# Performance work log

Hardware: AMD Instinct MI355X
Metric: run time of the kernel (lower is better)

The kernel has to match this reference:

```python
import jax, jax.numpy as jnp
import numpy as np

N, D = 512, 256          # n candidates, span_emb_size
R = 4                    # num relation types / etypes
FF = 512                 # mention_linker_ffnn_size, depth 1
L = 2                    # ieg_bignn_hidden_layers
DH = D // 2              # GraphConvolution output size


def setup_inputs() -> dict:
    key = jax.random.key(0)
    ks = jax.random.split(key, 12)
    s = lambda fan_in: 1.0 / np.sqrt(fan_in)
    return {
        "candidate_embs": jax.random.normal(ks[0], (N, D), jnp.float32),
        # relation scorer FFNN: 3D -> FF -> R
        "W_sc0": jax.random.normal(ks[1], (3 * D, FF), jnp.float32) * s(3 * D),
        "b_sc0": jnp.zeros((FF,), jnp.float32),
        "W_sc1": jax.random.normal(ks[2], (FF, R), jnp.float32) * s(FF),
        "b_sc1": jnp.zeros((R,), jnp.float32),
        # BiGCN: per-layer, per-relation fw/bw GraphConvolution D -> D//2
        "W_fw": jax.random.normal(ks[3], (L, R, D, DH), jnp.float32) * s(D),
        "b_fw": jnp.zeros((L, R, DH), jnp.float32),
        "W_bw": jax.random.normal(ks[4], (L, R, D, DH), jnp.float32) * s(D),
        "b_bw": jnp.zeros((L, R, DH), jnp.float32),
        # per-layer linear1: D -> D
        "W_lin": jax.random.normal(ks[5], (L, D, D), jnp.float32) * s(D),
        "b_lin": jnp.zeros((L, D), jnp.float32),
    }


def reference(candidate_embs, W_sc0, b_sc0, W_sc1, b_sc1,
              W_fw, b_fw, W_bw, b_bw, W_lin, b_lin):
    n, d = candidate_embs.shape
    # --- get_pair_embs: [n, n, 3d] = cat(src, target, src*target) ---
    src = jnp.broadcast_to(candidate_embs[None, :, :], (n, n, d))   # row i varies j
    tgt = jnp.broadcast_to(candidate_embs[:, None, :], (n, n, d))
    pair = jnp.concatenate([src, tgt, src * tgt], axis=-1)          # [n, n, 3d]
    # --- relation scorer FFNN (ReLU hidden, dropout=0 at inference) ---
    h = jax.nn.relu(jnp.einsum('ijk,kf->ijf', pair, W_sc0) + b_sc0)
    scores = jnp.einsum('ijf,fr->ijr', h, W_sc1) + b_sc1            # [n, n, R]
    probs = jax.nn.softmax(scores, axis=-1)
    # --- adjs_from_preds: detach, zero diagonal; bw = fw^T ---
    probs = jax.lax.stop_gradient(probs)
    A = jnp.moveaxis(probs, -1, 0)                                   # [R, n, n]
    eye = jnp.eye(n, dtype=bool)
    A = jnp.where(eye[None, :, :], 0.0, A)
    AT = jnp.swapaxes(A, 1, 2)
    # --- BiGCN: L layers of multi-relation bi-directional GCN ---
    x = candidate_embs
    for l in range(L):
        sup_fw = jnp.einsum('nd,rde->rne', x, W_fw[l])               # [R, n, DH]
        sup_bw = jnp.einsum('nd,rde->rne', x, W_bw[l])
        fw = jnp.einsum('rij,rje->rie', A, sup_fw) + b_fw[l][:, None, :]
        bw = jnp.einsum('rij,rje->rie', AT, sup_bw) + b_bw[l][:, None, :]
        outs = jnp.concatenate([bw, fw], axis=-1)                    # [R, n, D]
        x = jax.nn.relu(outs.sum(axis=0)) @ W_lin[l] + b_lin[l] + x  # residual
    return x
```

## Files before the change

kernel.cpp:

```cpp
#include <hip/hip_runtime.h>
#include <hip/hip_bf16.h>

using f32x4  = __attribute__((ext_vector_type(4))) float;
using bf16x8 = __attribute__((ext_vector_type(8))) short;

__device__ __forceinline__ unsigned short f2bf(float f) {
    union { __hip_bfloat16 h; unsigned short u; } cv;
    cv.h = __float2bfloat16(f);
    return cv.u;
}
__device__ __forceinline__ unsigned int pack2bf(float lo, float hi) {
    float2 t; t.x = lo; t.y = hi;
    union { __hip_bfloat162 h; unsigned int u; } cv;
    cv.h = __float22bfloat162_rn(t);
    return cv.u;
}

__global__ __launch_bounds__(512) void prep_uv_kernel(
        const float* __restrict__ E, const float* __restrict__ Wsc0, const float* __restrict__ bsc0,
        const float* __restrict__ Wfw, const float* __restrict__ bfw,
        const float* __restrict__ Wbw, const float* __restrict__ bbw,
        const float* __restrict__ Wlin,
        unsigned short* __restrict__ E16, unsigned short* __restrict__ W0p,
        unsigned short* __restrict__ WcatT, unsigned short* __restrict__ WlinT,
        float* __restrict__ bsumS, float* __restrict__ Upk, float* __restrict__ V) {
    __shared__ float sE[8][256];
    if (blockIdx.x < 512) {
        const int NE = 131072, NW0 = 131072, NCAT = 524288, NLIN = 131072;
        const int total = NE + NW0 + NCAT + NLIN + 512;
        for (int idx = blockIdx.x * 512 + threadIdx.x; idx < total; idx += 512 * 512) {
            int t = idx;
            if (t < NE) { E16[t] = f2bf(E[t]); continue; }
            t -= NE;
            if (t < NW0) {
                int e = t & 7, lane = (t >> 3) & 63, kk = (t >> 9) & 7, nb = (t >> 12) & 3, w = (t >> 14) & 7;
                int fcol = w * 64 + nb * 16 + (lane & 15);
                int k = kk * 32 + (lane >> 4) * 8 + e;
                W0p[t] = f2bf(Wsc0[(512 + k) * 512 + fcol]);
                continue;
            }
            t -= NW0;
            if (t < NCAT) {
                int e = t & 127, k = (t >> 7) & 255, r = (t >> 15) & 3, d = (t >> 17) & 1, l = t >> 18;
                const float* src = (d == 0) ? Wfw : Wbw;
                float v = src[((l * 4 + r) * 256 + k) * 128 + e];
                WcatT[(l * 1024 + d * 512 + r * 128 + e) * 256 + k] = f2bf(v);
                continue;
            }
            t -= NCAT;
            if (t < NLIN) {
                int d = t & 255, f = (t >> 8) & 255, l = t >> 16;
                WlinT[(l * 256 + d) * 256 + f] = f2bf(Wlin[(l * 256 + f) * 256 + d]);
                continue;
            }
            t -= NLIN;
            {
                int f = t & 255, l = t >> 8;
                float s = 0.f;
                if (f < 128) { for (int r = 0; r < 4; ++r) s += bbw[(l * 4 + r) * 128 + f]; }
                else         { for (int r = 0; r < 4; ++r) s += bfw[(l * 4 + r) * 128 + (f - 128)]; }
                bsumS[l * 256 + f] = s;
            }
        }
    } else {
        int j0 = (blockIdx.x - 512) * 8;
        int tid = threadIdx.x;
        for (int t = tid; t < 2048; t += 512) sE[t >> 8][t & 255] = E[j0 * 256 + t];
        __syncthreads();
        int f = tid;
        float u[8] = {0,0,0,0,0,0,0,0}, v[8] = {0,0,0,0,0,0,0,0};
        for (int k = 0; k < 256; ++k) {
            float wa = Wsc0[k * 512 + f];
            float wb = Wsc0[(256 + k) * 512 + f];
#pragma unroll
            for (int jj = 0; jj < 8; ++jj) { u[jj] += sE[jj][k] * wa; v[jj] += sE[jj][k] * wb; }
        }
        float b0f = bsc0[f];
        int w = f >> 6, nb = (f >> 4) & 3, l15 = f & 15;
#pragma unroll
        for (int jj = 0; jj < 8; ++jj) {
            int j = j0 + jj;
            int j0b = j >> 6, mb = (j >> 4) & 3, lane = ((j >> 2) & 3) * 16 + l15, reg = j & 3;
            Upk[((((j0b * 8 + w) * 4 + mb) * 4 + nb) * 64 + lane) * 4 + reg] = u[jj] + b0f;
            V[j * 512 + f] = v[jj];
        }
    }
}

__global__ __launch_bounds__(512, 4) void pair_kernel(
    const float* __restrict__ E, const unsigned short* __restrict__ W0p,
    const float* __restrict__ Upk, const float* __restrict__ V,
    const float* __restrict__ W1, const float* __restrict__ b1,
    unsigned short* __restrict__ A16) {

    __shared__ unsigned short prodL[64 * 256];
    __shared__ float partial2[64 * 36];
    __shared__ float scoresL[64 * 4];

    const int i = blockIdx.x;
    const int j0b = blockIdx.y;
    const int j0 = j0b * 64;
    const int tid = threadIdx.x;
    const int lane = tid & 63;
    const int w = tid >> 6;
    const int l15 = lane & 15, l4 = lane >> 4;

    float Vv[4];
#pragma unroll
    for (int nb = 0; nb < 4; ++nb) Vv[nb] = V[i * 512 + w * 64 + nb * 16 + l15];
    const float4* Up4 = (const float4*)Upk;
    f32x4 acc[4][4];
#pragma unroll
    for (int mb = 0; mb < 4; ++mb)
#pragma unroll
        for (int nb = 0; nb < 4; ++nb) {
            float4 uv_ = Up4[(((j0b * 8 + w) * 4 + mb) * 4 + nb) * 64 + lane];
            acc[mb][nb][0] = uv_.x + Vv[nb];
            acc[mb][nb][1] = uv_.y + Vv[nb];
            acc[mb][nb][2] = uv_.z + Vv[nb];
            acc[mb][nb][3] = uv_.w + Vv[nb];
        }

    {
        int m = tid >> 3;
        const float4* ej = (const float4*)(E + (j0 + m) * 256);
        const float4* ei = (const float4*)(E + i * 256);
        char* base = (char*)prodL;
#pragma unroll
        for (int c = 0; c < 8; ++c) {
            int q = (tid & 7) + c * 8;
            float4 a = ej[q], b = ei[q];
            uint2 val;
            val.x = pack2bf(a.x * b.x, a.y * b.y);
            val.y = pack2bf(a.z * b.z, a.w * b.w);
            int byteoff = m * 512 + ((q * 8) ^ ((m & 7) << 4));
            *(uint2*)(base + byteoff) = val;
        }
    }
    __syncthreads();

    const char* pbase = (const char*)prodL;
    const bf16x8* Wp8 = (const bf16x8*)W0p;
#pragma unroll
    for (int kk = 0; kk < 8; ++kk) {
        bf16x8 afr[4], bfr[4];
#pragma unroll
        for (int mb = 0; mb < 4; ++mb) {
            int row = mb * 16 + l15;
            int off = row * 512 + ((kk * 64 + l4 * 16) ^ ((row & 7) << 4));
            afr[mb] = *(const bf16x8*)(pbase + off);
        }
#pragma unroll
        for (int nb = 0; nb < 4; ++nb)
            bfr[nb] = Wp8[((w * 4 + nb) * 8 + kk) * 64 + lane];
#pragma unroll
        for (int mb = 0; mb < 4; ++mb)
#pragma unroll
            for (int nb = 0; nb < 4; ++nb)
                acc[mb][nb] = __builtin_amdgcn_mfma_f32_16x16x32_bf16(afr[mb], bfr[nb], acc[mb][nb], 0, 0, 0);
    }

    float4 w1v[4];
#pragma unroll
    for (int nb = 0; nb < 4; ++nb) w1v[nb] = *(const float4*)(W1 + (w * 64 + nb * 16 + l15) * 4);
#pragma unroll
    for (int mb = 0; mb < 4; ++mb) {
        float s2[4][4];
#pragma unroll
        for (int reg = 0; reg < 4; ++reg) {
            s2[reg][0] = 0.f; s2[reg][1] = 0.f; s2[reg][2] = 0.f; s2[reg][3] = 0.f;
#pragma unroll
            for (int nb = 0; nb < 4; ++nb) {
                float h = fmaxf(acc[mb][nb][reg], 0.f);
                s2[reg][0] += h * w1v[nb].x;
                s2[reg][1] += h * w1v[nb].y;
                s2[reg][2] += h * w1v[nb].z;
                s2[reg][3] += h * w1v[nb].w;
            }
        }
#pragma unroll
        for (int reg = 0; reg < 4; ++reg)
#pragma unroll
            for (int r = 0; r < 4; ++r) {
                float vs = s2[reg][r];
                vs += __shfl_xor(vs, 1);
                vs += __shfl_xor(vs, 2);
                vs += __shfl_xor(vs, 4);
                vs += __shfl_xor(vs, 8);
                s2[reg][r] = vs;
            }
#pragma unroll
        for (int reg = 0; reg < 4; ++reg)
#pragma unroll
            for (int r = 0; r < 4; ++r)
                if (l15 == r)
                    partial2[(mb * 16 + l4 * 4 + reg) * 36 + r * 9 + w] = s2[reg][r];
    }
    __syncthreads();
    if (tid < 256) {
        int m = tid >> 2, r = tid & 3;
        float sc = b1[r];
#pragma unroll
        for (int p = 0; p < 8; ++p) sc += partial2[m * 36 + r * 9 + p];
        scoresL[m * 4 + r] = sc;
    }
    __syncthreads();
    if (tid < 64) {
        int m = tid, j = j0 + m;
        float s0 = scoresL[m * 4 + 0], s1 = scoresL[m * 4 + 1];
        float sA = scoresL[m * 4 + 2], sB = scoresL[m * 4 + 3];
        float mx = fmaxf(fmaxf(s0, s1), fmaxf(sA, sB));
        float e0 = __expf(s0 - mx), e1 = __expf(s1 - mx), e2 = __expf(sA - mx), e3 = __expf(sB - mx);
        float inv = 1.f / (e0 + e1 + e2 + e3);
        float p_[4] = {e0 * inv, e1 * inv, e2 * inv, e3 * inv};
        if (j == i) { p_[0] = p_[1] = p_[2] = p_[3] = 0.f; }
#pragma unroll
        for (int r = 0; r < 4; ++r)
            A16[(r * 512 + i) * 512 + j] = f2bf(p_[r]);
    }
}

template<int K>
__device__ __forceinline__ void stageP(unsigned short* lds, const unsigned short* g, int ldg, int tid) {
    constexpr int SLOTS = K / 8;
#pragma unroll
    for (int it = 0; it < (32 * SLOTS) / 256; ++it) {
        int u = it * 256 + tid;
        int row = u / SLOTS, slot = u % SLOTS;
        uint4 v = *(const uint4*)(g + row * ldg + slot * 8);
        *(uint4*)((char*)lds + row * (K * 2) + ((slot * 16) ^ ((row & 7) << 4))) = v;
    }
}
template<int K>
__device__ __forceinline__ bf16x8 fragP(const unsigned short* lds, int row, int kc, int l4) {
    return *(const bf16x8*)((const char*)lds + row * (K * 2) + ((((kc * 4 + l4) * 16) ^ ((row & 7) << 4))));
}

__global__ __launch_bounds__(256) void c1_kernel(const unsigned short* __restrict__ WcatT,
                                                 const unsigned short* __restrict__ x16,
                                                 unsigned short* __restrict__ supT,
                                                 const unsigned short* __restrict__ A16,
                                                 unsigned short* __restrict__ AT16, int l) {
    __shared__ unsigned short lA[32 * 256], lB[32 * 256];
    int tid = threadIdx.x;
    if (blockIdx.y >= 16) {
        auto t = (unsigned short(*)[65])lA;
        int job = (blockIdx.y - 16) * 32 + blockIdx.x;
        int r = job >> 6, ty = (job >> 3) & 7, tx = job & 7;
        const unsigned short* src = A16 + (r * 512 + ty * 64) * 512 + tx * 64;
        unsigned short* dst = AT16 + (r * 512 + tx * 64) * 512 + ty * 64;
#pragma unroll
        for (int it = 0; it < 2; ++it) {
            int u = it * 256 + tid, row = u >> 3, c8 = (u & 7) * 8;
            uint4 v = *(const uint4*)(src + row * 512 + c8);
            const unsigned short* p = (const unsigned short*)&v;
#pragma unroll
            for (int e = 0; e < 8; ++e) t[c8 + e][row] = p[e];
        }
        __syncthreads();
#pragma unroll
        for (int it = 0; it < 2; ++it) {
            int u = it * 256 + tid, row = u >> 3, c8 = (u & 7) * 8;
            uint4 v; unsigned short* p = (unsigned short*)&v;
#pragma unroll
            for (int e = 0; e < 8; ++e) p[e] = t[row][c8 + e];
            *(uint4*)(dst + row * 512 + c8) = v;
        }
        return;
    }
    int c0 = blockIdx.x * 32, jt0 = blockIdx.y * 32;
    int lane = tid & 63, w = tid >> 6;
    int wr = (w >> 1) * 16, wc = (w & 1) * 16;
    int l15 = lane & 15, l4 = lane >> 4;
    stageP<256>(lA, WcatT + l * 262144 + c0 * 256, 256, tid);
    stageP<256>(lB, x16 + jt0 * 256, 256, tid);
    __syncthreads();
    f32x4 a0 = {0.f,0.f,0.f,0.f}, a1 = {0.f,0.f,0.f,0.f};
#pragma unroll
    for (int kc = 0; kc < 8; kc += 2) {
        a0 = __builtin_amdgcn_mfma_f32_16x16x32_bf16(fragP<256>(lA, wr + l15, kc, l4),
                                                     fragP<256>(lB, wc + l15, kc, l4), a0, 0, 0, 0);
        a1 = __builtin_amdgcn_mfma_f32_16x16x32_bf16(fragP<256>(lA, wr + l15, kc + 1, l4),
                                                     fragP<256>(lB, wc + l15, kc + 1, l4), a1, 0, 0, 0);
    }
    f32x4 acc = a0 + a1;
#pragma unroll
    for (int reg = 0; reg < 4; ++reg) {
        int c = c0 + wr + l4 * 4 + reg;
        int j = jt0 + wc + l15;
        supT[c * 512 + j] = f2bf(acc[reg]);
    }
}

__global__ __launch_bounds__(256) void c2_kernel(const unsigned short* __restrict__ A16,
                                                 const unsigned short* __restrict__ AT16,
                                                 const unsigned short* __restrict__ supT,
                                                 const float* __restrict__ bsumS,
                                                 unsigned short* __restrict__ relS, int l) {
    __shared__ unsigned short lA[32 * 512], lB[32 * 512];
    int i0 = blockIdx.x * 32, f0 = blockIdx.y * 32;
    bool bw = (f0 < 128);
    const unsigned short* Am = bw ? AT16 : A16;
    int e0 = bw ? f0 : (f0 - 128);
    int tid = threadIdx.x, lane = tid & 63, w = tid >> 6;
    int wr = (w >> 1) * 16, wc = (w & 1) * 16;
    int l15 = lane & 15, l4 = lane >> 4;
    f32x4 a0 = {0.f,0.f,0.f,0.f}, a1 = {0.f,0.f,0.f,0.f};
    for (int r = 0; r < 4; ++r) {
        if (r) __syncthreads();
        stageP<512>(lA, Am + (r * 512 + i0) * 512, 512, tid);
        stageP<512>(lB, supT + ((bw ? 512 : 0) + r * 128 + e0) * 512, 512, tid);
        __syncthreads();
#pragma unroll
        for (int kc = 0; kc < 16; kc += 2) {
            a0 = __builtin_amdgcn_mfma_f32_16x16x32_bf16(fragP<512>(lA, wr + l15, kc, l4),
                                                         fragP<512>(lB, wc + l15, kc, l4), a0, 0, 0, 0);
            a1 = __builtin_amdgcn_mfma_f32_16x16x32_bf16(fragP<512>(lA, wr + l15, kc + 1, l4),
                                                         fragP<512>(lB, wc + l15, kc + 1, l4), a1, 0, 0, 0);
        }
    }
    f32x4 acc = a0 + a1;
#pragma unroll
    for (int reg = 0; reg < 4; ++reg) {
        int ii = i0 + wr + l4 * 4 + reg;
        int f = f0 + wc + l15;
        relS[ii * 256 + f] = f2bf(fmaxf(acc[reg] + bsumS[l * 256 + f], 0.f));
    }
}

__global__ __launch_bounds__(256) void c3_kernel(const unsigned short* __restrict__ relS,
                                                 const unsigned short* __restrict__ WlinT,
                                                 const float* __restrict__ blin,
                                                 const float* __restrict__ xold,
                                                 float* __restrict__ xnew,
                                                 unsigned short* __restrict__ x16out, int l) {
    __shared__ unsigned short lA[32 * 256], lB[32 * 256];
    int i0 = blockIdx.x * 32, d0 = blockIdx.y * 32;
    int tid = threadIdx.x, lane = tid & 63, w = tid >> 6;
    int wr = (w >> 1) * 16, wc = (w & 1) * 16;
    int l15 = lane & 15, l4 = lane >> 4;
    stageP<256>(lA, relS + i0 * 256, 256, tid);
    stageP<256>(lB, WlinT + l * 65536 + d0 * 256, 256, tid);
    __syncthreads();
    f32x4 a0 = {0.f,0.f,0.f,0.f}, a1 = {0.f,0.f,0.f,0.f};
#pragma unroll
    for (int kc = 0; kc < 8; kc += 2) {
        a0 = __builtin_amdgcn_mfma_f32_16x16x32_bf16(fragP<256>(lA, wr + l15, kc, l4),
                                                     fragP<256>(lB, wc + l15, kc, l4), a0, 0, 0, 0);
        a1 = __builtin_amdgcn_mfma_f32_16x16x32_bf16(fragP<256>(lA, wr + l15, kc + 1, l4),
                                                     fragP<256>(lB, wc + l15, kc + 1, l4), a1, 0, 0, 0);
    }
    f32x4 acc = a0 + a1;
#pragma unroll
    for (int reg = 0; reg < 4; ++reg) {
        int ii = i0 + wr + l4 * 4 + reg;
        int dd = d0 + wc + l15;
        float vv = acc[reg] + blin[l * 256 + dd] + xold[ii * 256 + dd];
        xnew[ii * 256 + dd] = vv;
        x16out[ii * 256 + dd] = f2bf(vv);
    }
}

extern "C" void kernel_launch(void* const* d_in, const int* in_sizes, int n_in,
                              void* d_out, int out_size, void* d_ws, size_t ws_size,
                              hipStream_t stream) {
    const float* E    = (const float*)d_in[0];
    const float* Wsc0 = (const float*)d_in[1];
    const float* bsc0 = (const float*)d_in[2];
    const float* Wsc1 = (const float*)d_in[3];
    const float* bsc1 = (const float*)d_in[4];
    const float* Wfw  = (const float*)d_in[5];
    const float* bfw  = (const float*)d_in[6];
    const float* Wbw  = (const float*)d_in[7];
    const float* bbw  = (const float*)d_in[8];
    const float* Wlin = (const float*)d_in[9];
    const float* blin = (const float*)d_in[10];
    float* out = (float*)d_out;

    char* ws = (char*)d_ws;
    size_t off = 0;
    unsigned short* E16   = (unsigned short*)(ws + off); off += 512 * 256 * 2;
    unsigned short* W0p   = (unsigned short*)(ws + off); off += 512 * 256 * 2;
    unsigned short* WcatT = (unsigned short*)(ws + off); off += 2 * 1024 * 256 * 2;
    unsigned short* WlinT = (unsigned short*)(ws + off); off += 2 * 256 * 256 * 2;
    float* bsumS          = (float*)(ws + off);          off += 2 * 256 * 4;
    float* Upk            = (float*)(ws + off);          off += 512 * 512 * 4;
    float* V              = (float*)(ws + off);          off += 512 * 512 * 4;
    unsigned short* A16   = (unsigned short*)(ws + off); off += 4 * 512 * 512 * 2;
    unsigned short* AT16  = (unsigned short*)(ws + off); off += 4 * 512 * 512 * 2;
    unsigned short* supT  = (unsigned short*)(ws + off); off += 1024 * 512 * 2;
    unsigned short* relS  = (unsigned short*)(ws + off); off += 512 * 256 * 2;
    float* xf1            = (float*)(ws + off);          off += 512 * 256 * 4;
    unsigned short* x16_1 = (unsigned short*)(ws + off); off += 512 * 256 * 2;

    prep_uv_kernel<<<576, 512, 0, stream>>>(E, Wsc0, bsc0, Wfw, bfw, Wbw, bbw, Wlin,
                                            E16, W0p, WcatT, WlinT, bsumS, Upk, V);
    pair_kernel<<<dim3(512, 8), 512, 0, stream>>>(E, W0p, Upk, V, Wsc1, bsc1, A16);

    for (int l = 0; l < 2; ++l) {
        const unsigned short* xin16 = (l == 0) ? E16 : x16_1;
        const float* xoldf = (l == 0) ? E : xf1;
        float* xout = (l == 0) ? xf1 : out;
        c1_kernel<<<dim3(32, (l == 0) ? 24 : 16), 256, 0, stream>>>(WcatT, xin16, supT, A16, AT16, l);
        c2_kernel<<<dim3(16, 8), 256, 0, stream>>>(A16, AT16, supT, bsumS, relS, l);
        c3_kernel<<<dim3(16, 8), 256, 0, stream>>>(relS, WlinT, blin, xoldf, xout, x16_1, l);
    }
    (void)in_sizes; (void)n_in; (void)out_size; (void)ws_size;
}
```

Measured before the change: 223.9 us.

## Use MFMA for scorer output layer, bf16 U, split-K c2 with reduction in c3

The pair kernel's second FFNN layer (hidden to 4 relations) now runs on MFMA instead of scalar FMAs and shuffle reductions. Hidden activations are written to LDS as bf16, and W1 is padded into a 16-column bf16 fragment layout. The precomputed U term is stored as bf16 to halve its load traffic, and pair_kernel launch bounds are lowered to 3 waves/SIMD. The GCN aggregation kernel c2 is split across relation and K-half into 8 fp32 partial slices for more blocks, with c3 summing the slices, adding bias and ReLU. The costs are extra global traffic for the partials, more bf16 rounding, and added syncs in pair_kernel.

```diff
diff --git a/kernel.cpp b/kernel.cpp
--- a/kernel.cpp
+++ b/kernel.cpp
@@ -15,19 +15,24 @@
     cv.h = __float22bfloat162_rn(t);
     return cv.u;
 }
+__device__ __forceinline__ float bf2f(unsigned short u) {
+    return __uint_as_float((unsigned)u << 16);
+}
 
 __global__ __launch_bounds__(512) void prep_uv_kernel(
         const float* __restrict__ E, const float* __restrict__ Wsc0, const float* __restrict__ bsc0,
+        const float* __restrict__ Wsc1,
         const float* __restrict__ Wfw, const float* __restrict__ bfw,
         const float* __restrict__ Wbw, const float* __restrict__ bbw,
         const float* __restrict__ Wlin,
         unsigned short* __restrict__ E16, unsigned short* __restrict__ W0p,
         unsigned short* __restrict__ WcatT, unsigned short* __restrict__ WlinT,
-        float* __restrict__ bsumS, float* __restrict__ Upk, float* __restrict__ V) {
+        float* __restrict__ bsumS, unsigned short* __restrict__ Upk,
+        float* __restrict__ V, unsigned short* __restrict__ W1p) {
     __shared__ float sE[8][256];
     if (blockIdx.x < 512) {
-        const int NE = 131072, NW0 = 131072, NCAT = 524288, NLIN = 131072;
-        const int total = NE + NW0 + NCAT + NLIN + 512;
+        const int NE = 131072, NW0 = 131072, NCAT = 524288, NLIN = 131072, NW1P = 8192;
+        const int total = NE + NW0 + NCAT + NLIN + NW1P + 512;
         for (int idx = blockIdx.x * 512 + threadIdx.x; idx < total; idx += 512 * 512) {
             int t = idx;
             if (t < NE) { E16[t] = f2bf(E[t]); continue; }
@@ -54,6 +59,14 @@
                 continue;
             }
             t -= NLIN;
+            if (t < NW1P) {
+                int e = t & 7, lane = (t >> 3) & 63, kk = t >> 9;
+                int f = kk * 32 + (lane >> 4) * 8 + e;
+                int r = lane & 15;
+                W1p[t] = (r < 4) ? f2bf(Wsc1[f * 4 + r]) : (unsigned short)0;
+                continue;
+            }
+            t -= NW1P;
             {
                 int f = t & 255, l = t >> 8;
                 float s = 0.f;
@@ -80,26 +93,26 @@
 #pragma unroll
         for (int jj = 0; jj < 8; ++jj) {
             int j = j0 + jj;
-            int j0b = j >> 6, mb = (j >> 4) & 3, lane = ((j >> 2) & 3) * 16 + l15, reg = j & 3;
-            Upk[((((j0b * 8 + w) * 4 + mb) * 4 + nb) * 64 + lane) * 4 + reg] = u[jj] + b0f;
+            int jt = j >> 6, mb = (j >> 4) & 3, lane = ((j >> 2) & 3) * 16 + l15, reg = j & 3;
+            Upk[(((((jt * 8 + w) * 4 + mb) * 4 + nb) * 64 + lane) * 4 + reg)] = f2bf(u[jj] + b0f);
             V[j * 512 + f] = v[jj];
         }
     }
 }
 
-__global__ __launch_bounds__(512, 4) void pair_kernel(
+__global__ __launch_bounds__(512, 3) void pair_kernel(
     const float* __restrict__ E, const unsigned short* __restrict__ W0p,
-    const float* __restrict__ Upk, const float* __restrict__ V,
-    const float* __restrict__ W1, const float* __restrict__ b1,
+    const unsigned short* __restrict__ Upk, const float* __restrict__ V,
+    const unsigned short* __restrict__ W1p, const float* __restrict__ b1,
     unsigned short* __restrict__ A16) {
 
     __shared__ unsigned short prodL[64 * 256];
-    __shared__ float partial2[64 * 36];
+    __shared__ float Spart[8 * 64 * 5];
     __shared__ float scoresL[64 * 4];
 
     const int i = blockIdx.x;
-    const int j0b = blockIdx.y;
-    const int j0 = j0b * 64;
+    const int jt = blockIdx.y;
+    const int j0 = jt * 64;
     const int tid = threadIdx.x;
     const int lane = tid & 63;
     const int w = tid >> 6;
@@ -108,17 +121,17 @@
     float Vv[4];
 #pragma unroll
     for (int nb = 0; nb < 4; ++nb) Vv[nb] = V[i * 512 + w * 64 + nb * 16 + l15];
-    const float4* Up4 = (const float4*)Upk;
     f32x4 acc[4][4];
 #pragma unroll
     for (int mb = 0; mb < 4; ++mb)
 #pragma unroll
         for (int nb = 0; nb < 4; ++nb) {
-            float4 uv_ = Up4[(((j0b * 8 + w) * 4 + mb) * 4 + nb) * 64 + lane];
-            acc[mb][nb][0] = uv_.x + Vv[nb];
-            acc[mb][nb][1] = uv_.y + Vv[nb];
-            acc[mb][nb][2] = uv_.z + Vv[nb];
-            acc[mb][nb][3] = uv_.w + Vv[nb];
+            int idx4 = (((jt * 8 + w) * 4 + mb) * 4 + nb) * 64 + lane;
+            ushort4 uq = ((const ushort4*)Upk)[idx4];
+            acc[mb][nb][0] = bf2f(uq.x) + Vv[nb];
+            acc[mb][nb][1] = bf2f(uq.y) + Vv[nb];
+            acc[mb][nb][2] = bf2f(uq.z) + Vv[nb];
+            acc[mb][nb][3] = bf2f(uq.w) + Vv[nb];
         }
 
     {
@@ -160,48 +173,55 @@
                 acc[mb][nb] = __builtin_amdgcn_mfma_f32_16x16x32_bf16(afr[mb], bfr[nb], acc[mb][nb], 0, 0, 0);
     }
 
-    float4 w1v[4];
-#pragma unroll
-    for (int nb = 0; nb < 4; ++nb) w1v[nb] = *(const float4*)(W1 + (w * 64 + nb * 16 + l15) * 4);
-#pragma unroll
-    for (int mb = 0; mb < 4; ++mb) {
-        float s2[4][4];
-#pragma unroll
-        for (int reg = 0; reg < 4; ++reg) {
-            s2[reg][0] = 0.f; s2[reg][1] = 0.f; s2[reg][2] = 0.f; s2[reg][3] = 0.f;
+    __syncthreads();
+    char* hb = (char*)prodL;
+    const bf16x8* W1p8 = (const bf16x8*)W1p;
+    f32x4 accS[4];
+#pragma unroll
+    for (int q = 0; q < 4; ++q) accS[q] = (f32x4){0.f, 0.f, 0.f, 0.f};
+
+#pragma unroll
+    for (int p = 0; p < 2; ++p) {
+#pragma unroll
+        for (int mbl = 0; mbl < 2; ++mbl) {
 #pragma unroll
             for (int nb = 0; nb < 4; ++nb) {
-                float h = fmaxf(acc[mb][nb][reg], 0.f);
-                s2[reg][0] += h * w1v[nb].x;
-                s2[reg][1] += h * w1v[nb].y;
-                s2[reg][2] += h * w1v[nb].z;
-                s2[reg][3] += h * w1v[nb].w;
-            }
-        }
-#pragma unroll
-        for (int reg = 0; reg < 4; ++reg)
-#pragma unroll
-            for (int r = 0; r < 4; ++r) {
-                float vs = s2[reg][r];
-                vs += __shfl_xor(vs, 1);
-                vs += __shfl_xor(vs, 2);
-                vs += __shfl_xor(vs, 4);
-                vs += __shfl_xor(vs, 8);
-                s2[reg][r] = vs;
-            }
-#pragma unroll
-        for (int reg = 0; reg < 4; ++reg)
-#pragma unroll
-            for (int r = 0; r < 4; ++r)
-                if (l15 == r)
-                    partial2[(mb * 16 + l4 * 4 + reg) * 36 + r * 9 + w] = s2[reg][r];
+                int col = w * 64 + nb * 16 + l15;
+#pragma unroll
+                for (int reg = 0; reg < 4; ++reg) {
+                    int rl = mbl * 16 + l4 * 4 + reg;
+                    float hv = fmaxf(acc[p * 2 + mbl][nb][reg], 0.f);
+                    *(unsigned short*)(hb + rl * 1024 + ((col * 2) ^ ((rl & 7) << 4))) = f2bf(hv);
+                }
+            }
+        }
+        __syncthreads();
+#pragma unroll
+        for (int mbl = 0; mbl < 2; ++mbl) {
+            int rl = mbl * 16 + l15;
+#pragma unroll
+            for (int kkl = 0; kkl < 2; ++kkl) {
+                int kk = w * 2 + kkl;
+                bf16x8 ha = *(const bf16x8*)(hb + rl * 1024 + ((kk * 64 + l4 * 16) ^ ((rl & 7) << 4)));
+                accS[p * 2 + mbl] = __builtin_amdgcn_mfma_f32_16x16x32_bf16(ha, W1p8[kk * 64 + lane], accS[p * 2 + mbl], 0, 0, 0);
+            }
+        }
+        __syncthreads();
+    }
+
+    if (l15 < 4) {
+#pragma unroll
+        for (int q = 0; q < 4; ++q)
+#pragma unroll
+            for (int reg = 0; reg < 4; ++reg)
+                Spart[(w * 64 + q * 16 + l4 * 4 + reg) * 5 + l15] = accS[q][reg];
     }
     __syncthreads();
     if (tid < 256) {
         int m = tid >> 2, r = tid & 3;
         float sc = b1[r];
 #pragma unroll
-        for (int p = 0; p < 8; ++p) sc += partial2[m * 36 + r * 9 + p];
+        for (int p8 = 0; p8 < 8; ++p8) sc += Spart[(p8 * 64 + m) * 5 + r];
         scoresL[m * 4 + r] = sc;
     }
     __syncthreads();
@@ -229,6 +249,15 @@
         int row = u / SLOTS, slot = u % SLOTS;
         uint4 v = *(const uint4*)(g + row * ldg + slot * 8);
         *(uint4*)((char*)lds + row * (K * 2) + ((slot * 16) ^ ((row & 7) << 4))) = v;
+    }
+}
+__device__ __forceinline__ void stage64(unsigned short* lds, const unsigned short* g, int ldg, int tid) {
+#pragma unroll
+    for (int it = 0; it < 8; ++it) {
+        int u = it * 256 + tid;
+        int row = u >> 5, slot = u & 31;
+        uint4 v = *(const uint4*)(g + row * ldg + slot * 8);
+        *(uint4*)((char*)lds + row * 512 + ((slot * 16) ^ ((row & 7) << 4))) = v;
     }
 }
 template<int K>
@@ -295,40 +324,49 @@
 __global__ __launch_bounds__(256) void c2_kernel(const unsigned short* __restrict__ A16,
                                                  const unsigned short* __restrict__ AT16,
                                                  const unsigned short* __restrict__ supT,
+                                                 float* __restrict__ Pc2) {
+    __shared__ unsigned short lA[64 * 256], lB[64 * 256];
+    int i0 = blockIdx.x * 64, f0 = blockIdx.y * 64;
+    int s = blockIdx.z, r = s >> 1, kh = s & 1;
+    bool bw = (f0 < 128);
+    int e0 = bw ? f0 : (f0 - 128);
+    const unsigned short* Am = bw ? AT16 : A16;
+    int tid = threadIdx.x, lane = tid & 63, w = tid >> 6;
+    int wr = (w >> 1) * 32, wc = (w & 1) * 32;
+    int l15 = lane & 15, l4 = lane >> 4;
+    stage64(lA, Am + (r * 512 + i0) * 512 + kh * 256, 512, tid);
+    stage64(lB, supT + ((bw ? 512 : 0) + r * 128 + e0) * 512 + kh * 256, 512, tid);
+    __syncthreads();
+    f32x4 acc[2][2];
+#pragma unroll
+    for (int a_ = 0; a_ < 2; ++a_)
+#pragma unroll
+        for (int b_ = 0; b_ < 2; ++b_) acc[a_][b_] = (f32x4){0.f, 0.f, 0.f, 0.f};
+#pragma unroll
+    for (int kc = 0; kc < 8; ++kc) {
+        bf16x8 af[2], bf_[2];
+#pragma unroll
+        for (int mb = 0; mb < 2; ++mb) af[mb] = fragP<256>(lA, wr + mb * 16 + l15, kc, l4);
+#pragma unroll
+        for (int nb = 0; nb < 2; ++nb) bf_[nb] = fragP<256>(lB, wc + nb * 16 + l15, kc, l4);
+#pragma unroll
+        for (int mb = 0; mb < 2; ++mb)
+#pragma unroll
+            for (int nb = 0; nb < 2; ++nb)
+                acc[mb][nb] = __builtin_amdgcn_mfma_f32_16x16x32_bf16(af[mb], bf_[nb], acc[mb][nb], 0, 0, 0);
+    }
+    float* dst = Pc2 + s * 131072;
+#pragma unroll
+    for (int mb = 0; mb < 2; ++mb)
+#pragma unroll
+        for (int nb = 0; nb < 2; ++nb)
+#pragma unroll
+            for (int reg = 0; reg < 4; ++reg)
+                dst[(i0 + wr + mb * 16 + l4 * 4 + reg) * 256 + f0 + wc + nb * 16 + l15] = acc[mb][nb][reg];
+}
+
+__global__ __launch_bounds__(256) void c3_kernel(const float* __restrict__ Pc2,
                                                  const float* __restrict__ bsumS,
-                                                 unsigned short* __restrict__ relS, int l) {
-    __shared__ unsigned short lA[32 * 512], lB[32 * 512];
-    int i0 = blockIdx.x * 32, f0 = blockIdx.y * 32;
-    bool bw = (f0 < 128);
-    const unsigned short* Am = bw ? AT16 : A16;
-    int e0 = bw ? f0 : (f0 - 128);
-    int tid = threadIdx.x, lane = tid & 63, w = tid >> 6;
-    int wr = (w >> 1) * 16, wc = (w & 1) * 16;
-    int l15 = lane & 15, l4 = lane >> 4;
-    f32x4 a0 = {0.f,0.f,0.f,0.f}, a1 = {0.f,0.f,0.f,0.f};
-    for (int r = 0; r < 4; ++r) {
-        if (r) __syncthreads();
-        stageP<512>(lA, Am + (r * 512 + i0) * 512, 512, tid);
-        stageP<512>(lB, supT + ((bw ? 512 : 0) + r * 128 + e0) * 512, 512, tid);
-        __syncthreads();
-#pragma unroll
-        for (int kc = 0; kc < 16; kc += 2) {
-            a0 = __builtin_amdgcn_mfma_f32_16x16x32_bf16(fragP<512>(lA, wr + l15, kc, l4),
-                                                         fragP<512>(lB, wc + l15, kc, l4), a0, 0, 0, 0);
-            a1 = __builtin_amdgcn_mfma_f32_16x16x32_bf16(fragP<512>(lA, wr + l15, kc + 1, l4),
-                                                         fragP<512>(lB, wc + l15, kc + 1, l4), a1, 0, 0, 0);
-        }
-    }
-    f32x4 acc = a0 + a1;
-#pragma unroll
-    for (int reg = 0; reg < 4; ++reg) {
-        int ii = i0 + wr + l4 * 4 + reg;
-        int f = f0 + wc + l15;
-        relS[ii * 256 + f] = f2bf(fmaxf(acc[reg] + bsumS[l * 256 + f], 0.f));
-    }
-}
-
-__global__ __launch_bounds__(256) void c3_kernel(const unsigned short* __restrict__ relS,
                                                  const unsigned short* __restrict__ WlinT,
                                                  const float* __restrict__ blin,
                                                  const float* __restrict__ xold,
@@ -339,7 +377,28 @@
     int tid = threadIdx.x, lane = tid & 63, w = tid >> 6;
     int wr = (w >> 1) * 16, wc = (w & 1) * 16;
     int l15 = lane & 15, l4 = lane >> 4;
-    stageP<256>(lA, relS + i0 * 256, 256, tid);
+#pragma unroll
+    for (int g = 0; g < 4; ++g) {
+        int u = g * 256 + tid;
+        int row = u >> 5, k8 = (u & 31) * 8;
+        float s[8] = {0,0,0,0,0,0,0,0};
+#pragma unroll
+        for (int s8 = 0; s8 < 8; ++s8) {
+            const float4* p = (const float4*)(Pc2 + s8 * 131072 + (i0 + row) * 256 + k8);
+            float4 a = p[0], b = p[1];
+            s[0] += a.x; s[1] += a.y; s[2] += a.z; s[3] += a.w;
+            s[4] += b.x; s[5] += b.y; s[6] += b.z; s[7] += b.w;
+        }
+        uint4 v;
+        unsigned* vp = (unsigned*)&v;
+#pragma unroll
+        for (int e2 = 0; e2 < 4; ++e2) {
+            float lo = fmaxf(s[e2 * 2] + bsumS[l * 256 + k8 + e2 * 2], 0.f);
+            float hi = fmaxf(s[e2 * 2 + 1] + bsumS[l * 256 + k8 + e2 * 2 + 1], 0.f);
+            vp[e2] = pack2bf(lo, hi);
+        }
+        *(uint4*)((char*)lA + row * 512 + ((k8 * 2) ^ ((row & 7) << 4))) = v;
+    }
     stageP<256>(lB, WlinT + l * 65536 + d0 * 256, 256, tid);
     __syncthreads();
     f32x4 a0 = {0.f,0.f,0.f,0.f}, a1 = {0.f,0.f,0.f,0.f};
@@ -384,26 +443,27 @@
     unsigned short* WcatT = (unsigned short*)(ws + off); off += 2 * 1024 * 256 * 2;
     unsigned short* WlinT = (unsigned short*)(ws + off); off += 2 * 256 * 256 * 2;
     float* bsumS          = (float*)(ws + off);          off += 2 * 256 * 4;
-    float* Upk            = (float*)(ws + off);          off += 512 * 512 * 4;
+    unsigned short* Upk   = (unsigned short*)(ws + off); off += 512 * 512 * 2;
     float* V              = (float*)(ws + off);          off += 512 * 512 * 4;
+    unsigned short* W1p   = (unsigned short*)(ws + off); off += 16 * 64 * 8 * 2;
     unsigned short* A16   = (unsigned short*)(ws + off); off += 4 * 512 * 512 * 2;
     unsigned short* AT16  = (unsigned short*)(ws + off); off += 4 * 512 * 512 * 2;
     unsigned short* supT  = (unsigned short*)(ws + off); off += 1024 * 512 * 2;
-    unsigned short* relS  = (unsigned short*)(ws + off); off += 512 * 256 * 2;
+    float* Pc2            = (float*)(ws + off);          off += 8 * 512 * 256 * 4;
     float* xf1            = (float*)(ws + off);          off += 512 * 256 * 4;
     unsigned short* x16_1 = (unsigned short*)(ws + off); off += 512 * 256 * 2;
 
-    prep_uv_kernel<<<576, 512, 0, stream>>>(E, Wsc0, bsc0, Wfw, bfw, Wbw, bbw, Wlin,
-                                            E16, W0p, WcatT, WlinT, bsumS, Upk, V);
-    pair_kernel<<<dim3(512, 8), 512, 0, stream>>>(E, W0p, Upk, V, Wsc1, bsc1, A16);
+    prep_uv_kernel<<<576, 512, 0, stream>>>(E, Wsc0, bsc0, Wsc1, Wfw, bfw, Wbw, bbw, Wlin,
+                                            E16, W0p, WcatT, WlinT, bsumS, Upk, V, W1p);
+    pair_kernel<<<dim3(512, 8), 512, 0, stream>>>(E, W0p, Upk, V, W1p, bsc1, A16);
 
     for (int l = 0; l < 2; ++l) {
         const unsigned short* xin16 = (l == 0) ? E16 : x16_1;
         const float* xoldf = (l == 0) ? E : xf1;
         float* xout = (l == 0) ? xf1 : out;
         c1_kernel<<<dim3(32, (l == 0) ? 24 : 16), 256, 0, stream>>>(WcatT, xin16, supT, A16, AT16, l);
-        c2_kernel<<<dim3(16, 8), 256, 0, stream>>>(A16, AT16, supT, bsumS, relS, l);
-        c3_kernel<<<dim3(16, 8), 256, 0, stream>>>(relS, WlinT, blin, xoldf, xout, x16_1, l);
+        c2_kernel<<<dim3(8, 4, 8), 256, 0, stream>>>(A16, AT16, supT, Pc2);
+        c3_kernel<<<dim3(16, 8), 256, 0, stream>>>(Pc2, bsumS, WlinT, blin, xoldf, xout, x16_1, l);
     }
     (void)in_sizes; (void)n_in; (void)out_size; (void)ws_size;
 }
```

Result: faster. 212.7 us (-5.0%).
